# Optimization experiments

Measured on AMD Instinct MI355X. Metric: run time of the kernel, lower is better.

The kernel has to match this reference:

```python
import jax, jax.numpy as jnp
import numpy as np
from jax import lax

B, H, W, Q, C = 2, 96, 96, 30000, 64
DIMS = [C * 9 + 4, 256, 256, 256, 256, 3]  # imnet MLP


def setup_inputs() -> dict:
    key = jax.random.key(0)
    ks = jax.random.split(key, 20)
    d = {}
    d["inp"] = jax.random.normal(ks[0], (B, 3, H, W), jnp.float32)
    d["coord"] = jax.random.uniform(ks[1], (B, Q, 2), jnp.float32) * 2.0 - 1.0
    d["cell"] = jax.random.uniform(ks[2], (B, Q, 2), jnp.float32) * (2.0 / 256.0)
    d["conv_w"] = jax.random.normal(ks[3], (C, 3, 3, 3), jnp.float32) * 0.1
    d["conv_b"] = jnp.zeros((C,), jnp.float32)
    for i in range(5):
        fan_in = DIMS[i]
        d[f"w{i}"] = jax.random.normal(ks[4 + i], (DIMS[i], DIMS[i + 1]), jnp.float32) / np.sqrt(fan_in)
        d[f"b{i}"] = jnp.zeros((DIMS[i + 1],), jnp.float32)
    return d


def _liif_forward(inp, coord, cell, conv_w, conv_b, ws, bs):
    # encoder: 3x3 conv + tanh (gen_feat)
    feat = lax.conv_general_dilated(inp, conv_w, (1, 1), "SAME",
                                    dimension_numbers=("NCHW", "OIHW", "NCHW"))
    feat = jnp.tanh(feat + conv_b[None, :, None, None])  # [B,C,H,W]
    b, c, h, w = feat.shape

    # feat_unfold: F.unfold(feat, 3, padding=1) -> [B, C*9, H, W]
    pad = jnp.pad(feat, ((0, 0), (0, 0), (1, 1), (1, 1)))
    patches = jnp.stack([pad[:, :, i:i + h, j:j + w] for i in range(3) for j in range(3)], axis=2)
    fu = patches.reshape(b, c * 9, h, w).transpose(0, 2, 3, 1)  # [B,H,W,9C]

    # local ensemble offsets
    offsets = jnp.array([[-1., -1.], [-1., 1.], [1., -1.], [1., 1.]], jnp.float32)
    rad = jnp.array([1.0 / h, 1.0 / w], jnp.float32)  # 2/r/2
    eps = 1e-6
    ec = coord[None] + (offsets * rad)[:, None, None, :] + eps  # [4,B,Q,2]
    ec = jnp.clip(ec, -1 + 1e-10, 1 - 1e-10)

    # grid_sample nearest, align_corners=False: ix = ((x+1)*size - 1)/2, round
    iy = jnp.clip(jnp.round((ec[..., 0] + 1) * h / 2 - 0.5).astype(jnp.int32), 0, h - 1)
    ix = jnp.clip(jnp.round((ec[..., 1] + 1) * w / 2 - 0.5).astype(jnp.int32), 0, w - 1)
    b_idx = jnp.arange(b)[None, :, None]  # [1,B,1]
    q_feat = fu[b_idx, iy, ix]  # [4,B,Q,9C]

    # feat_coord (make_coord): pixel-center coords in [-1,1]
    yc = (-1.0 + (2.0 * jnp.arange(h, dtype=jnp.float32) + 1.0) / h)
    xc = (-1.0 + (2.0 * jnp.arange(w, dtype=jnp.float32) + 1.0) / w)
    fc = jnp.stack(jnp.meshgrid(yc, xc, indexing="ij"), axis=-1)  # [H,W,2]
    q_coord = fc[iy, ix]  # [4,B,Q,2]

    scale = jnp.array([h, w], jnp.float32)
    rel_coord = (coord[None] - q_coord) * scale  # [4,B,Q,2]
    rel_cell = cell * scale  # [B,Q,2]

    x = jnp.concatenate(
        [q_feat, rel_coord, jnp.broadcast_to(rel_cell[None], rel_coord.shape)], axis=-1)  # [4,B,Q,580]

    # imnet MLP
    for wi, bi in zip(ws[:-1], bs[:-1]):
        x = jax.nn.relu(x @ wi + bi)
    x = x @ ws[-1] + bs[-1]  # [4,B,Q,3]

    areas = jnp.abs(jnp.prod(rel_coord, axis=-1, keepdims=True)) + 1e-9
    areas = areas / jnp.sum(areas, axis=0, keepdims=True)
    areas = areas[::-1]  # swap diagonal ensemble weights

    out = jnp.sum(x * areas, axis=0)  # [B,Q,3]
    return jnp.tanh(out) * 1.01  # fat_tanh(eps=0.01)


def reference(inp, coord, cell, conv_w, conv_b, w0, b0, w1, b1, w2, b2, w3, b3, w4, b4):
    return _liif_forward(inp, coord, cell, conv_w, conv_b,
                         [w0, w1, w2, w3, w4], [b0, b1, b2, b3, b4])
```

## Files before the change

### kernel.cpp

```cpp
#include <hip/hip_runtime.h>


typedef _Float16 half8   __attribute__((ext_vector_type(8)));
typedef _Float16 half4v  __attribute__((ext_vector_type(4)));
typedef _Float16 half2v  __attribute__((ext_vector_type(2)));
typedef float    float4v __attribute__((ext_vector_type(4)));
typedef float    floatx16 __attribute__((ext_vector_type(16)));

__device__ __forceinline__ _Float16 to_h(float v) {
  return (_Float16)fminf(fmaxf(v, -60000.0f), 60000.0f);
}

#define NQ 30000
#define QT 469
#define QTP 472

__global__ void prep_kernel(const float* __restrict__ w0,
                            const float* __restrict__ w1,
                            const float* __restrict__ w2,
                            const float* __restrict__ w3,
                            const float* __restrict__ w4,
                            _Float16* __restrict__ p0, _Float16* __restrict__ p1,
                            _Float16* __restrict__ p2, _Float16* __restrict__ p3,
                            _Float16* __restrict__ p4) {
  int idx = blockIdx.x * 256 + threadIdx.x;
  if (idx < 18944) {
    int kb = idx >> 8, n = idx & 255;
    half8 hv;
#pragma unroll
    for (int i = 0; i < 8; ++i) {
      int f = kb * 8 + i;
      float v = 0.0f;
      if (f < 576)      v = w0[((f & 63) * 9 + (f >> 6)) * 256 + n];
      else if (f < 580) v = w0[f * 256 + n];
      hv[i] = (_Float16)v;
    }
    *(half8*)(p0 + idx * 8) = hv;
  } else if (idx < 43520) {
    int j = idx - 18944;
    int l = j >> 13;
    int j2 = j & 8191;
    int kb = j2 >> 8, n = j2 & 255;
    const float* w = (l == 0) ? w1 : (l == 1) ? w2 : w3;
    _Float16* p = (l == 0) ? p1 : (l == 1) ? p2 : p3;
    half8 hv;
#pragma unroll
    for (int i = 0; i < 8; ++i)
      hv[i] = (_Float16)w[(kb * 8 + i) * 256 + n];
    *(half8*)(p + j2 * 8) = hv;
  } else if (idx < 44032) {
    int j = idx - 43520;
    int kb = j >> 4, n = j & 15;
    half8 hv;
#pragma unroll
    for (int i = 0; i < 8; ++i) {
      float v = (n < 3) ? w4[(kb * 8 + i) * 3 + n] : 0.0f;
      hv[i] = (_Float16)v;
    }
    *(half8*)(p4 + j * 8) = hv;
  }
}

__global__ void conv_kernel(const float* __restrict__ inp,
                            const float* __restrict__ cw,
                            const float* __restrict__ cb,
                            _Float16* __restrict__ P) {
  __shared__ __align__(16) float s_w[1728];
  __shared__ __align__(16) float s_b[64];
  for (int i = threadIdx.x; i < 1728; i += 256) s_w[i] = cw[i];
  if (threadIdx.x < 64) s_b[threadIdx.x] = cb[threadIdx.x];
  __syncthreads();
  int tid = blockIdx.x * 256 + threadIdx.x;
  if (tid >= 2 * 98 * 98) return;
  int b = tid / 9604;
  int rem = tid % 9604;
  int yy = rem / 98, xx = rem % 98;
  alignas(16) _Float16 outv[64];
  if (yy == 0 || yy == 97 || xx == 0 || xx == 97) {
#pragma unroll
    for (int c = 0; c < 64; ++c) outv[c] = (_Float16)0.0f;
  } else {
    int y = yy - 1, x = xx - 1;
    float win[27];
#pragma unroll
    for (int ci = 0; ci < 3; ++ci)
#pragma unroll
      for (int ky = 0; ky < 3; ++ky)
#pragma unroll
        for (int kx = 0; kx < 3; ++kx) {
          int yi = y + ky - 1, xi = x + kx - 1;
          float v = 0.0f;
          if (yi >= 0 && yi < 96 && xi >= 0 && xi < 96)
            v = inp[((b * 3 + ci) * 96 + yi) * 96 + xi];
          win[ci * 9 + ky * 3 + kx] = v;
        }
    for (int co = 0; co < 64; ++co) {
      float acc = s_b[co];
#pragma unroll
      for (int k = 0; k < 27; ++k) acc = fmaf(win[k], s_w[co * 27 + k], acc);
      outv[co] = (_Float16)tanhf(acc);
    }
  }
  _Float16* dst = P + tid * 64;
#pragma unroll
  for (int j = 0; j < 8; ++j) ((half8*)dst)[j] = ((const half8*)outv)[j];
}

__global__ __launch_bounds__(256, 2) void gmat_kernel(
    const _Float16* __restrict__ P,
    const _Float16* __restrict__ wp0,
    _Float16* __restrict__ G) {
  __shared__ __align__(16) _Float16 s_p[3][98][68];

  const int t    = threadIdx.x;
  const int lane = t & 63;
  const int wv   = t >> 6;
  const int ln32 = lane & 31;
  const int hi   = lane >> 5;
  const int blk  = blockIdx.x;
  const int bb   = (blk & 4) >> 2;
  const int mh   = (blk >> 3) & 1;
  const int y    = (blk >> 4) * 4 + (blk & 3);
  const int mt   = mh * 4 + wv;

  const int rowbase = (bb * 98 + y) * 98 * 64;
  for (int j = t; j < 2352; j += 256) {
    int row = j / 784;
    int jr  = j - row * 784;
    half8 v = *(const half8*)(P + rowbase + row * 6272 + jr * 8);
    *(half8*)(&s_p[row][jr >> 3][(jr & 7) * 8]) = v;
  }
  __syncthreads();

  const _Float16* wb0 = wp0 + (hi * 256 + mt * 32 + ln32) * 8;

  floatx16 acc[3];
#pragma unroll
  for (int nt = 0; nt < 3; ++nt) acc[nt] = (floatx16)(0.0f);

  half8 afA, afB;
  afA = *(const half8*)(wb0);
  afB = *(const half8*)(wb0 + 4096);

#pragma unroll 1
  for (int s = 0; s < 36; s += 2) {
    {
      const int patch = s >> 2;
      const int py = patch / 3, px = patch % 3;
      const int cb = ((s & 3) << 4) + hi * 8;
      half8 bf[3];
#pragma unroll
      for (int nt = 0; nt < 3; ++nt)
        bf[nt] = *(const half8*)(&s_p[py][nt * 32 + ln32 + px][cb]);
#pragma unroll
      for (int nt = 0; nt < 3; ++nt)
        acc[nt] = __builtin_amdgcn_mfma_f32_32x32x16_f16(afA, bf[nt], acc[nt], 0, 0, 0);
      const int sp = (s + 2 <= 35) ? (s + 2) : 35;
      afA = *(const half8*)(wb0 + sp * 4096);
    }
    {
      const int s1 = s + 1;
      const int patch = s1 >> 2;
      const int py = patch / 3, px = patch % 3;
      const int cb = ((s1 & 3) << 4) + hi * 8;
      half8 bf[3];
#pragma unroll
      for (int nt = 0; nt < 3; ++nt)
        bf[nt] = *(const half8*)(&s_p[py][nt * 32 + ln32 + px][cb]);
#pragma unroll
      for (int nt = 0; nt < 3; ++nt)
        acc[nt] = __builtin_amdgcn_mfma_f32_32x32x16_f16(afB, bf[nt], acc[nt], 0, 0, 0);
      const int sp = (s + 3 <= 35) ? (s + 3) : 35;
      afB = *(const half8*)(wb0 + sp * 4096);
    }
  }
  const int gybase = ((bb * 98 + y) * 98) * 256;
#pragma unroll
  for (int nt = 0; nt < 3; ++nt) {
    half8 c0, c1;
#pragma unroll
    for (int j = 0; j < 8; ++j) {
      c0[j] = (_Float16)acc[nt][j];
      c1[j] = (_Float16)acc[nt][8 + j];
    }
    _Float16* ga = G + gybase + (nt * 32 + ln32) * 256 + mt * 32 + hi * 16;
    *(half8*)(ga)     = c0;
    *(half8*)(ga + 8) = c1;
  }
}

__device__ __forceinline__ void writeback32(floatx16 (&acc)[2][4],
                                            const float* __restrict__ sb,
                                            _Float16 (*s_h)[264],
                                            int wv, int ln32, int hi) {
#pragma unroll
  for (int mt2 = 0; mt2 < 2; ++mt2) {
    const int mb = wv * 64 + mt2 * 32 + 4 * hi;
#pragma unroll
    for (int g = 0; g < 4; ++g) {
      const int m0 = mb + 8 * g;
      float b0 = sb[m0], b1 = sb[m0 + 1], b2 = sb[m0 + 2], b3 = sb[m0 + 3];
#pragma unroll
      for (int nt2 = 0; nt2 < 4; ++nt2) {
        const int n = nt2 * 32 + ln32;
        float v0 = fmaxf(acc[mt2][nt2][4 * g + 0] + b0, 0.0f);
        float v1 = fmaxf(acc[mt2][nt2][4 * g + 1] + b1, 0.0f);
        float v2 = fmaxf(acc[mt2][nt2][4 * g + 2] + b2, 0.0f);
        float v3 = fmaxf(acc[mt2][nt2][4 * g + 3] + b3, 0.0f);
        half2v lo  = __builtin_bit_cast(half2v, __builtin_amdgcn_cvt_pkrtz(v0, v1));
        half2v hi2 = __builtin_bit_cast(half2v, __builtin_amdgcn_cvt_pkrtz(v2, v3));
        half4v hv;
        hv[0] = lo[0]; hv[1] = lo[1]; hv[2] = hi2[0]; hv[3] = hi2[1];
        *(half4v*)(&s_h[n][m0]) = hv;
      }
    }
  }
}

__device__ __forceinline__ void layer256(const _Float16* __restrict__ wbl,
                                         _Float16 (*s_h)[264],
                                         int ln32, int hi,
                                         floatx16 (&acc)[2][4]) {
#pragma unroll
  for (int mt2 = 0; mt2 < 2; ++mt2)
#pragma unroll
    for (int nt2 = 0; nt2 < 4; ++nt2) acc[mt2][nt2] = (floatx16)(0.0f);
  half8 afA[2], afB[2], bfA[4], bfB[4];
  afA[0] = *(const half8*)(wbl);
  afA[1] = *(const half8*)(wbl + 256);
  afB[0] = *(const half8*)(wbl + 4096);
  afB[1] = *(const half8*)(wbl + 4096 + 256);
#pragma unroll
  for (int nt2 = 0; nt2 < 4; ++nt2) {
    bfA[nt2] = *(const half8*)(&s_h[nt2 * 32 + ln32][hi * 8]);
    bfB[nt2] = *(const half8*)(&s_h[nt2 * 32 + ln32][16 + hi * 8]);
  }
#pragma unroll 1
  for (int s = 0; s < 16; s += 2) {
#pragma unroll
    for (int mt2 = 0; mt2 < 2; ++mt2)
#pragma unroll
      for (int nt2 = 0; nt2 < 4; ++nt2)
        acc[mt2][nt2] = __builtin_amdgcn_mfma_f32_32x32x16_f16(
            afA[mt2], bfA[nt2], acc[mt2][nt2], 0, 0, 0);
    {
      const int sc = (s + 2 < 16) ? (s + 2) : 0;
      const int sw = (s + 2 < 16) ? (s + 2) : 15;
      afA[0] = *(const half8*)(wbl + sw * 4096);
      afA[1] = *(const half8*)(wbl + sw * 4096 + 256);
#pragma unroll
      for (int nt2 = 0; nt2 < 4; ++nt2)
        bfA[nt2] = *(const half8*)(&s_h[nt2 * 32 + ln32][sc * 16 + hi * 8]);
    }
#pragma unroll
    for (int mt2 = 0; mt2 < 2; ++mt2)
#pragma unroll
      for (int nt2 = 0; nt2 < 4; ++nt2)
        acc[mt2][nt2] = __builtin_amdgcn_mfma_f32_32x32x16_f16(
            afB[mt2], bfB[nt2], acc[mt2][nt2], 0, 0, 0);
    {
      const int sc = (s + 3 < 16) ? (s + 3) : 0;
      const int sw = (s + 3 < 16) ? (s + 3) : 15;
      afB[0] = *(const half8*)(wbl + sw * 4096);
      afB[1] = *(const half8*)(wbl + sw * 4096 + 256);
#pragma unroll
      for (int nt2 = 0; nt2 < 4; ++nt2)
        bfB[nt2] = *(const half8*)(&s_h[nt2 * 32 + ln32][sc * 16 + hi * 8]);
    }
  }
}

__global__ __launch_bounds__(256, 2) void liif_main(
    const float* __restrict__ coord, const float* __restrict__ cell,
    const float* __restrict__ bias0, const float* __restrict__ bias1,
    const float* __restrict__ bias2, const float* __restrict__ bias3,
    const float* __restrict__ bias4,
    const _Float16* __restrict__ G,
    const _Float16* __restrict__ wp0, const _Float16* __restrict__ wp1,
    const _Float16* __restrict__ wp2, const _Float16* __restrict__ wp3,
    const _Float16* __restrict__ wp4,
    float* __restrict__ out) {
  __shared__ __align__(16) int      s_pix[4][64];
  __shared__ __align__(16) float    s_area[4][64];
  __shared__ __align__(16) _Float16 s_ext[4][64][8];
  __shared__ __align__(16) float    s_bias[1028];
  __shared__ __align__(16) float    s_out[128][4];
  __shared__ __align__(16) float    s_num[64][4];
  __shared__ __align__(16) _Float16 s_h[128][264];

  const int t   = threadIdx.x;
  const int blk = blockIdx.x;
  const int bb  = (blk & 4) >> 2;
  const int tile = (blk >> 3) * 4 + (blk & 3);
  const int q0  = tile * 64;

  for (int i = t; i < 1027; i += 256) {
    float v;
    if (i < 256)       v = bias0[i];
    else if (i < 512)  v = bias1[i - 256];
    else if (i < 768)  v = bias2[i - 512];
    else if (i < 1024) v = bias3[i - 768];
    else               v = bias4[i - 1024];
    s_bias[i] = v;
  }

  if (t < 64) {
    int q = q0 + t;
    bool valid = q < NQ;
    float c0 = 0.f, c1 = 0.f, e0 = 0.f, e1 = 0.f;
    if (valid) {
      int base = (bb * NQ + q) * 2;
      c0 = coord[base]; c1 = coord[base + 1];
      e0 = cell[base];  e1 = cell[base + 1];
    }
    float rc0 = e0 * 96.0f, rc1 = e1 * 96.0f;
#pragma unroll
    for (int o = 0; o < 4; ++o) {
      float oy = (o < 2) ? -1.0f : 1.0f;
      float ox = (o & 1) ? 1.0f : -1.0f;
      float ec0 = (c0 + oy * (1.0f / 96.0f)) + 1e-6f;
      float ec1 = (c1 + ox * (1.0f / 96.0f)) + 1e-6f;
      ec0 = fminf(fmaxf(ec0, -1.0f), 1.0f);
      ec1 = fminf(fmaxf(ec1, -1.0f), 1.0f);
      int iy = (int)rintf(((ec0 + 1.0f) * 96.0f) * 0.5f - 0.5f);
      int ix = (int)rintf(((ec1 + 1.0f) * 96.0f) * 0.5f - 0.5f);
      iy = min(max(iy, 0), 95); ix = min(max(ix, 0), 95);
      float qc0 = -1.0f + (2.0f * (float)iy + 1.0f) / 96.0f;
      float qc1 = -1.0f + (2.0f * (float)ix + 1.0f) / 96.0f;
      float r0 = (c0 - qc0) * 96.0f;
      float r1 = (c1 - qc1) * 96.0f;
      s_pix[o][t]  = (bb * 98 + iy) * 98 + ix;
      s_area[o][t] = fabsf(r0 * r1) + 1e-9f;
      s_ext[o][t][0] = to_h(r0);  s_ext[o][t][1] = to_h(r1);
      s_ext[o][t][2] = to_h(rc0); s_ext[o][t][3] = to_h(rc1);
      s_ext[o][t][4] = (_Float16)0.0f; s_ext[o][t][5] = (_Float16)0.0f;
      s_ext[o][t][6] = (_Float16)0.0f; s_ext[o][t][7] = (_Float16)0.0f;
    }
    s_num[t][0] = 0.f; s_num[t][1] = 0.f; s_num[t][2] = 0.f; s_num[t][3] = 0.f;
  }
  __syncthreads();

  const int lane = t & 63;
  const int wv   = t >> 6;
  const int ln32 = lane & 31;
  const int hi   = lane >> 5;
  const int ln16 = lane & 15;
  const int lg   = lane >> 4;

  const _Float16* wb0 = wp0 + (hi * 256 + wv * 64 + ln32) * 8;
  const _Float16* wb1 = wp1 + (hi * 256 + wv * 64 + ln32) * 8;
  const _Float16* wb2 = wp2 + (hi * 256 + wv * 64 + ln32) * 8;
  const _Float16* wb3 = wp3 + (hi * 256 + wv * 64 + ln32) * 8;

#pragma unroll 1
  for (int p = 0; p < 2; ++p) {
    int pixr[4]; int eidx[4];
#pragma unroll
    for (int nt2 = 0; nt2 < 4; ++nt2) {
      int r = nt2 * 32 + ln32;
      int o = p * 2 + (r >> 6);
      int q = r & 63;
      pixr[nt2] = s_pix[o][q];
      eidx[nt2] = (o * 64 + q) * 8;
    }

    floatx16 acc[2][4];
#pragma unroll
    for (int mt2 = 0; mt2 < 2; ++mt2)
#pragma unroll
      for (int nt2 = 0; nt2 < 4; ++nt2) {
        const _Float16* ga = G + pixr[nt2] * 256 + (wv * 2 + mt2) * 32 + hi * 16;
        half8 g0 = *(const half8*)(ga);
        half8 g1 = *(const half8*)(ga + 8);
        floatx16 a;
#pragma unroll
        for (int j = 0; j < 8; ++j) {
          a[j]     = (float)g0[j];
          a[8 + j] = (float)g1[j];
        }
        acc[mt2][nt2] = a;
      }
    {
      half8 ae[2];
      ae[0] = *(const half8*)(wb0 + 36 * 4096);
      ae[1] = *(const half8*)(wb0 + 36 * 4096 + 256);
      half8 z = {(_Float16)0, (_Float16)0, (_Float16)0, (_Float16)0,
                 (_Float16)0, (_Float16)0, (_Float16)0, (_Float16)0};
      half8 bfe[4];
#pragma unroll
      for (int nt2 = 0; nt2 < 4; ++nt2)
        bfe[nt2] = (hi == 0) ? *(const half8*)(&s_ext[0][0][0] + eidx[nt2]) : z;
#pragma unroll
      for (int mt2 = 0; mt2 < 2; ++mt2)
#pragma unroll
        for (int nt2 = 0; nt2 < 4; ++nt2)
          acc[mt2][nt2] = __builtin_amdgcn_mfma_f32_32x32x16_f16(
              ae[mt2], bfe[nt2], acc[mt2][nt2], 0, 0, 0);
    }
    writeback32(acc, s_bias, s_h, wv, ln32, hi);
    __syncthreads();

    layer256(wb1, s_h, ln32, hi, acc);
    __syncthreads();
    writeback32(acc, s_bias + 256, s_h, wv, ln32, hi);
    __syncthreads();

    layer256(wb2, s_h, ln32, hi, acc);
    __syncthreads();
    writeback32(acc, s_bias + 512, s_h, wv, ln32, hi);
    __syncthreads();

    layer256(wb3, s_h, ln32, hi, acc);
    __syncthreads();
    writeback32(acc, s_bias + 768, s_h, wv, ln32, hi);
    __syncthreads();

    half8 af4 = *(const half8*)(wp4 + (lg * 16 + ln16) * 8);
    float4v a4[2];
    a4[0] = (float4v){0.f, 0.f, 0.f, 0.f};
    a4[1] = (float4v){0.f, 0.f, 0.f, 0.f};
#pragma unroll 1
    for (int s = 0; s < 8; ++s) {
      half8 afc = af4;
      if (s < 7)
        af4 = *(const half8*)(wp4 + (((s + 1) * 4 + lg) * 16 + ln16) * 8);
#pragma unroll
      for (int u = 0; u < 2; ++u) {
        int row = (2 * wv + u) * 16 + ln16;
        half8 bf = *(const half8*)(&s_h[row][s * 32 + lg * 8]);
        a4[u] = __builtin_amdgcn_mfma_f32_16x16x32_f16(afc, bf, a4[u], 0, 0, 0);
      }
    }
    if (lg == 0) {
#pragma unroll
      for (int u = 0; u < 2; ++u) {
        int row = (2 * wv + u) * 16 + ln16;
        *(float4v*)(&s_out[row][0]) = a4[u];
      }
    }
    __syncthreads();

    if (t < 64) {
      float a_lo = s_area[3 - 2 * p][t];
      float a_hi = s_area[2 - 2 * p][t];
#pragma unroll
      for (int j = 0; j < 3; ++j)
        s_num[t][j] += s_out[t][j] * a_lo + s_out[64 + t][j] * a_hi;
    }
  }

  if (t < 64) {
    int q = q0 + t;
    if (q < NQ) {
      float den = s_area[0][t] + s_area[1][t] + s_area[2][t] + s_area[3][t];
      int ob = (bb * NQ + q) * 3;
#pragma unroll
      for (int j = 0; j < 3; ++j) {
        float v = s_num[t][j] / den + s_bias[1024 + j];
        out[ob + j] = tanhf(v) * 1.01f;
      }
    }
  }
}

extern "C" void kernel_launch(void* const* d_in, const int* in_sizes, int n_in,
                              void* d_out, int out_size, void* d_ws, size_t ws_size,
                              hipStream_t stream) {
  const float* inp   = (const float*)d_in[0];
  const float* coord = (const float*)d_in[1];
  const float* cell  = (const float*)d_in[2];
  const float* cw    = (const float*)d_in[3];
  const float* cb    = (const float*)d_in[4];
  const float* w0    = (const float*)d_in[5];
  const float* b0    = (const float*)d_in[6];
  const float* w1    = (const float*)d_in[7];
  const float* b1    = (const float*)d_in[8];
  const float* w2    = (const float*)d_in[9];
  const float* b2    = (const float*)d_in[10];
  const float* w3    = (const float*)d_in[11];
  const float* b3    = (const float*)d_in[12];
  const float* w4    = (const float*)d_in[13];
  const float* b4    = (const float*)d_in[14];

  char* ws = (char*)d_ws;
  _Float16* P   = (_Float16*)(ws);
  _Float16* wp0 = (_Float16*)(ws + 2458624);
  _Float16* wp1 = (_Float16*)(ws + 2761728);
  _Float16* wp2 = (_Float16*)(ws + 2892800);
  _Float16* wp3 = (_Float16*)(ws + 3023872);
  _Float16* wp4 = (_Float16*)(ws + 3154944);
  _Float16* G   = (_Float16*)(ws + 3163136);
  float* outp = (float*)d_out;

  hipLaunchKernelGGL(prep_kernel, dim3(172), dim3(256), 0, stream,
                     w0, w1, w2, w3, w4, wp0, wp1, wp2, wp3, wp4);
  hipLaunchKernelGGL(conv_kernel, dim3(76), dim3(256), 0, stream, inp, cw, cb, P);
  hipLaunchKernelGGL(gmat_kernel, dim3(384), dim3(256), 0, stream, P, wp0, G);
  hipLaunchKernelGGL(liif_main, dim3(8 * (QTP / 4)), dim3(256), 0, stream,
                     coord, cell, b0, b1, b2, b3, b4,
                     G, wp0, wp1, wp2, wp3, wp4, outp);
}
```

Measured before the change: 267.0 us.

## Keep MLP activations in registers per wave instead of shared-memory staging

The main kernel is restructured so that each wave handles one ensemble offset for 32 queries and computes all 256 output channels itself. Hidden activations stay in registers and are repacked between layers with cross-half-wave shuffles, which removes the shared-memory activation buffer and most block-wide barriers. The cost is that every wave now streams the full weight matrices from global memory or cache per layer, and register pressure is much higher with 8 accumulator tiles plus 64 packed activation registers. The grid doubles because tiles shrink to 32 queries, and the final layer's weight packing is widened to 32 columns to fit a 32x32 MFMA.

```diff
diff --git a/kernel.cpp b/kernel.cpp
--- a/kernel.cpp
+++ b/kernel.cpp
@@ -2,18 +2,18 @@
 
 
 typedef _Float16 half8   __attribute__((ext_vector_type(8)));
-typedef _Float16 half4v  __attribute__((ext_vector_type(4)));
 typedef _Float16 half2v  __attribute__((ext_vector_type(2)));
 typedef float    float4v __attribute__((ext_vector_type(4)));
 typedef float    floatx16 __attribute__((ext_vector_type(16)));
+typedef unsigned uint4v  __attribute__((ext_vector_type(4)));
 
 __device__ __forceinline__ _Float16 to_h(float v) {
   return (_Float16)fminf(fmaxf(v, -60000.0f), 60000.0f);
 }
 
 #define NQ 30000
-#define QT 469
-#define QTP 472
+#define QT32 938
+#define QTP32 940
 
 __global__ void prep_kernel(const float* __restrict__ w0,
                             const float* __restrict__ w1,
@@ -48,13 +48,14 @@
     for (int i = 0; i < 8; ++i)
       hv[i] = (_Float16)w[(kb * 8 + i) * 256 + n];
     *(half8*)(p + j2 * 8) = hv;
-  } else if (idx < 44032) {
+  } else if (idx < 44544) {
     int j = idx - 43520;
-    int kb = j >> 4, n = j & 15;
+    int kb2 = j >> 5, n = j & 31;
     half8 hv;
 #pragma unroll
     for (int i = 0; i < 8; ++i) {
-      float v = (n < 3) ? w4[(kb * 8 + i) * 3 + n] : 0.0f;
+      int k = kb2 * 8 + i;
+      float v = (n < 3) ? w4[k * 3 + n] : 0.0f;
       hv[i] = (_Float16)v;
     }
     *(half8*)(p4 + j * 8) = hv;
@@ -189,83 +190,56 @@
   }
 }
 
-__device__ __forceinline__ void writeback32(floatx16 (&acc)[2][4],
-                                            const float* __restrict__ sb,
-                                            _Float16 (*s_h)[264],
-                                            int wv, int ln32, int hi) {
-#pragma unroll
-  for (int mt2 = 0; mt2 < 2; ++mt2) {
-    const int mb = wv * 64 + mt2 * 32 + 4 * hi;
+
+__device__ __forceinline__ void pack_h(floatx16 (&acc)[8],
+                                       const float* __restrict__ sb,
+                                       int hi, unsigned (&hb)[16][4]) {
+#pragma unroll
+  for (int mt = 0; mt < 8; ++mt) {
+    unsigned p0[4], p1[4];
 #pragma unroll
     for (int g = 0; g < 4; ++g) {
-      const int m0 = mb + 8 * g;
+      const int m0 = mt * 32 + 8 * g + 4 * hi;
       float b0 = sb[m0], b1 = sb[m0 + 1], b2 = sb[m0 + 2], b3 = sb[m0 + 3];
-#pragma unroll
-      for (int nt2 = 0; nt2 < 4; ++nt2) {
-        const int n = nt2 * 32 + ln32;
-        float v0 = fmaxf(acc[mt2][nt2][4 * g + 0] + b0, 0.0f);
-        float v1 = fmaxf(acc[mt2][nt2][4 * g + 1] + b1, 0.0f);
-        float v2 = fmaxf(acc[mt2][nt2][4 * g + 2] + b2, 0.0f);
-        float v3 = fmaxf(acc[mt2][nt2][4 * g + 3] + b3, 0.0f);
-        half2v lo  = __builtin_bit_cast(half2v, __builtin_amdgcn_cvt_pkrtz(v0, v1));
-        half2v hi2 = __builtin_bit_cast(half2v, __builtin_amdgcn_cvt_pkrtz(v2, v3));
-        half4v hv;
-        hv[0] = lo[0]; hv[1] = lo[1]; hv[2] = hi2[0]; hv[3] = hi2[1];
-        *(half4v*)(&s_h[n][m0]) = hv;
-      }
-    }
-  }
-}
-
-__device__ __forceinline__ void layer256(const _Float16* __restrict__ wbl,
-                                         _Float16 (*s_h)[264],
-                                         int ln32, int hi,
-                                         floatx16 (&acc)[2][4]) {
-#pragma unroll
-  for (int mt2 = 0; mt2 < 2; ++mt2)
-#pragma unroll
-    for (int nt2 = 0; nt2 < 4; ++nt2) acc[mt2][nt2] = (floatx16)(0.0f);
-  half8 afA[2], afB[2], bfA[4], bfB[4];
-  afA[0] = *(const half8*)(wbl);
-  afA[1] = *(const half8*)(wbl + 256);
-  afB[0] = *(const half8*)(wbl + 4096);
-  afB[1] = *(const half8*)(wbl + 4096 + 256);
-#pragma unroll
-  for (int nt2 = 0; nt2 < 4; ++nt2) {
-    bfA[nt2] = *(const half8*)(&s_h[nt2 * 32 + ln32][hi * 8]);
-    bfB[nt2] = *(const half8*)(&s_h[nt2 * 32 + ln32][16 + hi * 8]);
-  }
-#pragma unroll 1
-  for (int s = 0; s < 16; s += 2) {
-#pragma unroll
-    for (int mt2 = 0; mt2 < 2; ++mt2)
-#pragma unroll
-      for (int nt2 = 0; nt2 < 4; ++nt2)
-        acc[mt2][nt2] = __builtin_amdgcn_mfma_f32_32x32x16_f16(
-            afA[mt2], bfA[nt2], acc[mt2][nt2], 0, 0, 0);
-    {
-      const int sc = (s + 2 < 16) ? (s + 2) : 0;
-      const int sw = (s + 2 < 16) ? (s + 2) : 15;
-      afA[0] = *(const half8*)(wbl + sw * 4096);
-      afA[1] = *(const half8*)(wbl + sw * 4096 + 256);
-#pragma unroll
-      for (int nt2 = 0; nt2 < 4; ++nt2)
-        bfA[nt2] = *(const half8*)(&s_h[nt2 * 32 + ln32][sc * 16 + hi * 8]);
-    }
-#pragma unroll
-    for (int mt2 = 0; mt2 < 2; ++mt2)
-#pragma unroll
-      for (int nt2 = 0; nt2 < 4; ++nt2)
-        acc[mt2][nt2] = __builtin_amdgcn_mfma_f32_32x32x16_f16(
-            afB[mt2], bfB[nt2], acc[mt2][nt2], 0, 0, 0);
-    {
-      const int sc = (s + 3 < 16) ? (s + 3) : 0;
-      const int sw = (s + 3 < 16) ? (s + 3) : 15;
-      afB[0] = *(const half8*)(wbl + sw * 4096);
-      afB[1] = *(const half8*)(wbl + sw * 4096 + 256);
-#pragma unroll
-      for (int nt2 = 0; nt2 < 4; ++nt2)
-        bfB[nt2] = *(const half8*)(&s_h[nt2 * 32 + ln32][sc * 16 + hi * 8]);
+      float v0 = fmaxf(acc[mt][4 * g + 0] + b0, 0.0f);
+      float v1 = fmaxf(acc[mt][4 * g + 1] + b1, 0.0f);
+      float v2 = fmaxf(acc[mt][4 * g + 2] + b2, 0.0f);
+      float v3 = fmaxf(acc[mt][4 * g + 3] + b3, 0.0f);
+      p0[g] = __builtin_bit_cast(unsigned, __builtin_amdgcn_cvt_pkrtz(v0, v1));
+      p1[g] = __builtin_bit_cast(unsigned, __builtin_amdgcn_cvt_pkrtz(v2, v3));
+    }
+    unsigned s00 = hi ? p0[0] : p0[1];
+    unsigned s01 = hi ? p1[0] : p1[1];
+    unsigned s10 = hi ? p0[2] : p0[3];
+    unsigned s11 = hi ? p1[2] : p1[3];
+    unsigned r00 = __shfl_xor(s00, 32);
+    unsigned r01 = __shfl_xor(s01, 32);
+    unsigned r10 = __shfl_xor(s10, 32);
+    unsigned r11 = __shfl_xor(s11, 32);
+    hb[2 * mt][0]     = hi ? r00   : p0[0];
+    hb[2 * mt][1]     = hi ? r01   : p1[0];
+    hb[2 * mt][2]     = hi ? p0[1] : r00;
+    hb[2 * mt][3]     = hi ? p1[1] : r01;
+    hb[2 * mt + 1][0] = hi ? r10   : p0[2];
+    hb[2 * mt + 1][1] = hi ? r11   : p1[2];
+    hb[2 * mt + 1][2] = hi ? p0[3] : r10;
+    hb[2 * mt + 1][3] = hi ? p1[3] : r11;
+  }
+}
+
+__device__ __forceinline__ void layerR(const _Float16* __restrict__ wbase,
+                                       const unsigned (&hb)[16][4],
+                                       floatx16 (&acc)[8]) {
+#pragma unroll
+  for (int mt = 0; mt < 8; ++mt) acc[mt] = (floatx16)(0.0f);
+#pragma unroll
+  for (int kb = 0; kb < 16; ++kb) {
+    uint4v u = {hb[kb][0], hb[kb][1], hb[kb][2], hb[kb][3]};
+    half8 bf = __builtin_bit_cast(half8, u);
+#pragma unroll
+    for (int mt = 0; mt < 8; ++mt) {
+      half8 af = *(const half8*)(wbase + kb * 4096 + mt * 256);
+      acc[mt] = __builtin_amdgcn_mfma_f32_32x32x16_f16(af, bf, acc[mt], 0, 0, 0);
     }
   }
 }
@@ -280,19 +254,19 @@
     const _Float16* __restrict__ wp2, const _Float16* __restrict__ wp3,
     const _Float16* __restrict__ wp4,
     float* __restrict__ out) {
-  __shared__ __align__(16) int      s_pix[4][64];
-  __shared__ __align__(16) float    s_area[4][64];
-  __shared__ __align__(16) _Float16 s_ext[4][64][8];
-  __shared__ __align__(16) float    s_bias[1028];
-  __shared__ __align__(16) float    s_out[128][4];
-  __shared__ __align__(16) float    s_num[64][4];
-  __shared__ __align__(16) _Float16 s_h[128][264];
-
-  const int t   = threadIdx.x;
-  const int blk = blockIdx.x;
-  const int bb  = (blk & 4) >> 2;
+  __shared__ __align__(16) float s_bias[1028];
+  __shared__ __align__(16) float s_area[4][32];
+  __shared__ __align__(16) float s_o4[4][32][4];
+
+  const int t    = threadIdx.x;
+  const int lane = t & 63;
+  const int wv   = t >> 6;
+  const int ln32 = lane & 31;
+  const int hi   = lane >> 5;
+  const int blk  = blockIdx.x;
+  const int bb   = (blk & 4) >> 2;
   const int tile = (blk >> 3) * 4 + (blk & 3);
-  const int q0  = tile * 64;
+  const int q0   = tile * 32;
 
   for (int i = t; i < 1027; i += 256) {
     float v;
@@ -304,159 +278,103 @@
     s_bias[i] = v;
   }
 
-  if (t < 64) {
-    int q = q0 + t;
-    bool valid = q < NQ;
-    float c0 = 0.f, c1 = 0.f, e0 = 0.f, e1 = 0.f;
-    if (valid) {
-      int base = (bb * NQ + q) * 2;
-      c0 = coord[base]; c1 = coord[base + 1];
-      e0 = cell[base];  e1 = cell[base + 1];
-    }
-    float rc0 = e0 * 96.0f, rc1 = e1 * 96.0f;
-#pragma unroll
-    for (int o = 0; o < 4; ++o) {
-      float oy = (o < 2) ? -1.0f : 1.0f;
-      float ox = (o & 1) ? 1.0f : -1.0f;
-      float ec0 = (c0 + oy * (1.0f / 96.0f)) + 1e-6f;
-      float ec1 = (c1 + ox * (1.0f / 96.0f)) + 1e-6f;
-      ec0 = fminf(fmaxf(ec0, -1.0f), 1.0f);
-      ec1 = fminf(fmaxf(ec1, -1.0f), 1.0f);
-      int iy = (int)rintf(((ec0 + 1.0f) * 96.0f) * 0.5f - 0.5f);
-      int ix = (int)rintf(((ec1 + 1.0f) * 96.0f) * 0.5f - 0.5f);
-      iy = min(max(iy, 0), 95); ix = min(max(ix, 0), 95);
-      float qc0 = -1.0f + (2.0f * (float)iy + 1.0f) / 96.0f;
-      float qc1 = -1.0f + (2.0f * (float)ix + 1.0f) / 96.0f;
-      float r0 = (c0 - qc0) * 96.0f;
-      float r1 = (c1 - qc1) * 96.0f;
-      s_pix[o][t]  = (bb * 98 + iy) * 98 + ix;
-      s_area[o][t] = fabsf(r0 * r1) + 1e-9f;
-      s_ext[o][t][0] = to_h(r0);  s_ext[o][t][1] = to_h(r1);
-      s_ext[o][t][2] = to_h(rc0); s_ext[o][t][3] = to_h(rc1);
-      s_ext[o][t][4] = (_Float16)0.0f; s_ext[o][t][5] = (_Float16)0.0f;
-      s_ext[o][t][6] = (_Float16)0.0f; s_ext[o][t][7] = (_Float16)0.0f;
-    }
-    s_num[t][0] = 0.f; s_num[t][1] = 0.f; s_num[t][2] = 0.f; s_num[t][3] = 0.f;
-  }
+  const int q = q0 + ln32;
+  const bool valid = q < NQ;
+  float c0 = 0.f, c1 = 0.f, e0 = 0.f, e1 = 0.f;
+  if (valid) {
+    int base = (bb * NQ + q) * 2;
+    c0 = coord[base]; c1 = coord[base + 1];
+    e0 = cell[base];  e1 = cell[base + 1];
+  }
+  const float rc0 = e0 * 96.0f, rc1 = e1 * 96.0f;
+  const float oy = (wv < 2) ? -1.0f : 1.0f;
+  const float ox = (wv & 1) ? 1.0f : -1.0f;
+  float ec0 = (c0 + oy * (1.0f / 96.0f)) + 1e-6f;
+  float ec1 = (c1 + ox * (1.0f / 96.0f)) + 1e-6f;
+  ec0 = fminf(fmaxf(ec0, -1.0f), 1.0f);
+  ec1 = fminf(fmaxf(ec1, -1.0f), 1.0f);
+  int iy = (int)rintf(((ec0 + 1.0f) * 96.0f) * 0.5f - 0.5f);
+  int ix = (int)rintf(((ec1 + 1.0f) * 96.0f) * 0.5f - 0.5f);
+  iy = min(max(iy, 0), 95); ix = min(max(ix, 0), 95);
+  const float qc0 = -1.0f + (2.0f * (float)iy + 1.0f) / 96.0f;
+  const float qc1 = -1.0f + (2.0f * (float)ix + 1.0f) / 96.0f;
+  const float r0 = (c0 - qc0) * 96.0f;
+  const float r1 = (c1 - qc1) * 96.0f;
+  const int   pix = (bb * 98 + iy) * 98 + ix;
+  if (hi == 0) s_area[wv][ln32] = fabsf(r0 * r1) + 1e-9f;
   __syncthreads();
 
-  const int lane = t & 63;
-  const int wv   = t >> 6;
-  const int ln32 = lane & 31;
-  const int hi   = lane >> 5;
-  const int ln16 = lane & 15;
-  const int lg   = lane >> 4;
-
-  const _Float16* wb0 = wp0 + (hi * 256 + wv * 64 + ln32) * 8;
-  const _Float16* wb1 = wp1 + (hi * 256 + wv * 64 + ln32) * 8;
-  const _Float16* wb2 = wp2 + (hi * 256 + wv * 64 + ln32) * 8;
-  const _Float16* wb3 = wp3 + (hi * 256 + wv * 64 + ln32) * 8;
-
-#pragma unroll 1
-  for (int p = 0; p < 2; ++p) {
-    int pixr[4]; int eidx[4];
-#pragma unroll
-    for (int nt2 = 0; nt2 < 4; ++nt2) {
-      int r = nt2 * 32 + ln32;
-      int o = p * 2 + (r >> 6);
-      int q = r & 63;
-      pixr[nt2] = s_pix[o][q];
-      eidx[nt2] = (o * 64 + q) * 8;
-    }
-
-    floatx16 acc[2][4];
-#pragma unroll
-    for (int mt2 = 0; mt2 < 2; ++mt2)
-#pragma unroll
-      for (int nt2 = 0; nt2 < 4; ++nt2) {
-        const _Float16* ga = G + pixr[nt2] * 256 + (wv * 2 + mt2) * 32 + hi * 16;
-        half8 g0 = *(const half8*)(ga);
-        half8 g1 = *(const half8*)(ga + 8);
-        floatx16 a;
-#pragma unroll
-        for (int j = 0; j < 8; ++j) {
-          a[j]     = (float)g0[j];
-          a[8 + j] = (float)g1[j];
-        }
-        acc[mt2][nt2] = a;
-      }
-    {
-      half8 ae[2];
-      ae[0] = *(const half8*)(wb0 + 36 * 4096);
-      ae[1] = *(const half8*)(wb0 + 36 * 4096 + 256);
-      half8 z = {(_Float16)0, (_Float16)0, (_Float16)0, (_Float16)0,
+  floatx16 acc[8];
+#pragma unroll
+  for (int mt = 0; mt < 8; ++mt) {
+    const _Float16* ga = G + pix * 256 + mt * 32 + hi * 16;
+    half8 g0 = *(const half8*)(ga);
+    half8 g1 = *(const half8*)(ga + 8);
+    floatx16 a;
+#pragma unroll
+    for (int j = 0; j < 8; ++j) {
+      a[j]     = (float)g0[j];
+      a[8 + j] = (float)g1[j];
+    }
+    acc[mt] = a;
+  }
+  {
+    half8 bfe = {(_Float16)0, (_Float16)0, (_Float16)0, (_Float16)0,
                  (_Float16)0, (_Float16)0, (_Float16)0, (_Float16)0};
-      half8 bfe[4];
-#pragma unroll
-      for (int nt2 = 0; nt2 < 4; ++nt2)
-        bfe[nt2] = (hi == 0) ? *(const half8*)(&s_ext[0][0][0] + eidx[nt2]) : z;
-#pragma unroll
-      for (int mt2 = 0; mt2 < 2; ++mt2)
-#pragma unroll
-        for (int nt2 = 0; nt2 < 4; ++nt2)
-          acc[mt2][nt2] = __builtin_amdgcn_mfma_f32_32x32x16_f16(
-              ae[mt2], bfe[nt2], acc[mt2][nt2], 0, 0, 0);
-    }
-    writeback32(acc, s_bias, s_h, wv, ln32, hi);
-    __syncthreads();
-
-    layer256(wb1, s_h, ln32, hi, acc);
-    __syncthreads();
-    writeback32(acc, s_bias + 256, s_h, wv, ln32, hi);
-    __syncthreads();
-
-    layer256(wb2, s_h, ln32, hi, acc);
-    __syncthreads();
-    writeback32(acc, s_bias + 512, s_h, wv, ln32, hi);
-    __syncthreads();
-
-    layer256(wb3, s_h, ln32, hi, acc);
-    __syncthreads();
-    writeback32(acc, s_bias + 768, s_h, wv, ln32, hi);
-    __syncthreads();
-
-    half8 af4 = *(const half8*)(wp4 + (lg * 16 + ln16) * 8);
-    float4v a4[2];
-    a4[0] = (float4v){0.f, 0.f, 0.f, 0.f};
-    a4[1] = (float4v){0.f, 0.f, 0.f, 0.f};
-#pragma unroll 1
-    for (int s = 0; s < 8; ++s) {
-      half8 afc = af4;
-      if (s < 7)
-        af4 = *(const half8*)(wp4 + (((s + 1) * 4 + lg) * 16 + ln16) * 8);
-#pragma unroll
-      for (int u = 0; u < 2; ++u) {
-        int row = (2 * wv + u) * 16 + ln16;
-        half8 bf = *(const half8*)(&s_h[row][s * 32 + lg * 8]);
-        a4[u] = __builtin_amdgcn_mfma_f32_16x16x32_f16(afc, bf, a4[u], 0, 0, 0);
-      }
-    }
-    if (lg == 0) {
-#pragma unroll
-      for (int u = 0; u < 2; ++u) {
-        int row = (2 * wv + u) * 16 + ln16;
-        *(float4v*)(&s_out[row][0]) = a4[u];
-      }
-    }
-    __syncthreads();
-
-    if (t < 64) {
-      float a_lo = s_area[3 - 2 * p][t];
-      float a_hi = s_area[2 - 2 * p][t];
-#pragma unroll
-      for (int j = 0; j < 3; ++j)
-        s_num[t][j] += s_out[t][j] * a_lo + s_out[64 + t][j] * a_hi;
-    }
-  }
-
-  if (t < 64) {
-    int q = q0 + t;
-    if (q < NQ) {
-      float den = s_area[0][t] + s_area[1][t] + s_area[2][t] + s_area[3][t];
-      int ob = (bb * NQ + q) * 3;
+    if (hi == 0) {
+      bfe[0] = to_h(r0); bfe[1] = to_h(r1); bfe[2] = to_h(rc0); bfe[3] = to_h(rc1);
+    }
+    const _Float16* we = wp0 + 36 * 4096 + (hi * 256 + ln32) * 8;
+#pragma unroll
+    for (int mt = 0; mt < 8; ++mt) {
+      half8 ae = *(const half8*)(we + mt * 256);
+      acc[mt] = __builtin_amdgcn_mfma_f32_32x32x16_f16(ae, bfe, acc[mt], 0, 0, 0);
+    }
+  }
+
+  unsigned hb[16][4];
+  pack_h(acc, s_bias, hi, hb);
+
+  const _Float16* wbase1 = wp1 + (hi * 256 + ln32) * 8;
+  const _Float16* wbase2 = wp2 + (hi * 256 + ln32) * 8;
+  const _Float16* wbase3 = wp3 + (hi * 256 + ln32) * 8;
+
+  layerR(wbase1, hb, acc);
+  pack_h(acc, s_bias + 256, hi, hb);
+  layerR(wbase2, hb, acc);
+  pack_h(acc, s_bias + 512, hi, hb);
+  layerR(wbase3, hb, acc);
+  pack_h(acc, s_bias + 768, hi, hb);
+
+  floatx16 a4 = (floatx16)(0.0f);
+  {
+    const _Float16* w4base = wp4 + (hi * 32 + ln32) * 8;
+#pragma unroll
+    for (int kb = 0; kb < 16; ++kb) {
+      uint4v u = {hb[kb][0], hb[kb][1], hb[kb][2], hb[kb][3]};
+      half8 bf = __builtin_bit_cast(half8, u);
+      half8 af = *(const half8*)(w4base + kb * 512);
+      a4 = __builtin_amdgcn_mfma_f32_32x32x16_f16(af, bf, a4, 0, 0, 0);
+    }
+  }
+  if (hi == 0) {
+    s_o4[wv][ln32][0] = a4[0];
+    s_o4[wv][ln32][1] = a4[1];
+    s_o4[wv][ln32][2] = a4[2];
+  }
+  __syncthreads();
+
+  if (t < 32) {
+    int qq = q0 + t;
+    if (qq < NQ) {
+      float a0 = s_area[0][t], a1 = s_area[1][t], a2 = s_area[2][t], a3 = s_area[3][t];
+      float den = a0 + a1 + a2 + a3;
+      int ob = (bb * NQ + qq) * 3;
 #pragma unroll
       for (int j = 0; j < 3; ++j) {
-        float v = s_num[t][j] / den + s_bias[1024 + j];
+        float num = s_o4[0][t][j] * a3 + s_o4[1][t][j] * a2 +
+                    s_o4[2][t][j] * a1 + s_o4[3][t][j] * a0;
+        float v = num / den + s_bias[1024 + j];
         out[ob + j] = tanhf(v) * 1.01f;
       }
     }
@@ -489,14 +407,14 @@
   _Float16* wp2 = (_Float16*)(ws + 2892800);
   _Float16* wp3 = (_Float16*)(ws + 3023872);
   _Float16* wp4 = (_Float16*)(ws + 3154944);
-  _Float16* G   = (_Float16*)(ws + 3163136);
+  _Float16* G   = (_Float16*)(ws + 3171328);
   float* outp = (float*)d_out;
 
-  hipLaunchKernelGGL(prep_kernel, dim3(172), dim3(256), 0, stream,
+  hipLaunchKernelGGL(prep_kernel, dim3(174), dim3(256), 0, stream,
                      w0, w1, w2, w3, w4, wp0, wp1, wp2, wp3, wp4);
   hipLaunchKernelGGL(conv_kernel, dim3(76), dim3(256), 0, stream, inp, cw, cb, P);
   hipLaunchKernelGGL(gmat_kernel, dim3(384), dim3(256), 0, stream, P, wp0, G);
-  hipLaunchKernelGGL(liif_main, dim3(8 * (QTP / 4)), dim3(256), 0, stream,
+  hipLaunchKernelGGL(liif_main, dim3(8 * (QTP32 / 4)), dim3(256), 0, stream,
                      coord, cell, b0, b1, b2, b3, b4,
                      G, wp0, wp1, wp2, wp3, wp4, outp);
 }
```

Result: slower. 450.4 us (+68.7%).
